# Optimization experiments

Hardware: AMD Instinct MI355X
Metric: run time of the kernel (lower is better)

Reference implementation:

```python
import jax, jax.numpy as jnp
import numpy as np

NUM_HEADS = 16

def setup_inputs() -> dict:
    key = jax.random.key(0)
    ks = jax.random.split(key, 5)
    b, c, w, h = 2, 1024, 48, 48
    sc = 0.02
    return {
        "x": jax.random.normal(ks[0], (b, c, w, h), jnp.float32),
        "Wqkv": jax.random.normal(ks[1], (3 * c, c), jnp.float32) * sc,
        "bqkv": jax.random.normal(ks[2], (3 * c,), jnp.float32) * sc,
        "Wo": jax.random.normal(ks[3], (c, c), jnp.float32) * sc,
        "bo": jax.random.normal(ks[4], (c,), jnp.float32) * sc,
    }

def reference(x, Wqkv, bqkv, Wo, bo):
    b, c, w, h = x.shape
    n = NUM_HEADS
    hd = c // n
    s = w * h
    # [b,c,w,h] -> tokens [b, s, c]
    xs = x.transpose(0, 2, 3, 1).reshape(b, s, c)
    qkv = xs @ Wqkv.T + bqkv                       # [b, s, 3c]
    # rearrange 'b s (three n hd) -> three b n s hd'
    qkv = qkv.reshape(b, s, 3, n, hd).transpose(2, 0, 3, 1, 4)
    q, k, v = qkv[0], qkv[1], qkv[2]               # [b, n, s, hd]
    score = jnp.einsum('bnqh,bnkh->bnqk', q, k) / jnp.sqrt(jnp.float32(hd))
    # module uses a soft causal mask: subtract 10000 above the diagonal
    mask = 10000.0 * jnp.triu(jnp.ones((s, s), dtype=score.dtype), k=1)
    attn = jax.nn.softmax(score - mask, axis=-1)   # [b, n, s, s]
    z = jnp.einsum('bnqk,bnkh->bqnh', attn, v).reshape(b, s, c)
    out = z @ Wo.T + bo                            # [b, s, c]
    return out.reshape(b, w, h, c).transpose(0, 3, 1, 2)
```

## Files before the change

### kernel.cpp

```cpp
#include <hip/hip_runtime.h>

typedef __bf16 bf16;
typedef __bf16 bf16x8 __attribute__((ext_vector_type(8)));
typedef float floatx4 __attribute__((ext_vector_type(4)));
typedef float floatx16 __attribute__((ext_vector_type(16)));

static constexpr int S = 2304;
static constexpr int C = 1024;
static constexpr int NHEAD = 16;
static constexpr int HDIM = 64;
static constexpr int BATCH = 2;
static constexpr float QSCALE = 0.18033688011112042f;
static constexpr int QACC0 = 512;
static constexpr int NACCQ = S - QACC0;
static constexpr int NPART = 3;

__global__ __launch_bounds__(256) void k_convert(const float* __restrict__ src,
                                                 bf16* __restrict__ dst, int n8) {
  int i = blockIdx.x * 256 + threadIdx.x;
  if (i >= n8) return;
  float4 a = *(const float4*)(src + (size_t)i * 8);
  float4 b = *(const float4*)(src + (size_t)i * 8 + 4);
  bf16x8 o;
  o[0] = (bf16)a.x; o[1] = (bf16)a.y; o[2] = (bf16)a.z; o[3] = (bf16)a.w;
  o[4] = (bf16)b.x; o[5] = (bf16)b.y; o[6] = (bf16)b.z; o[7] = (bf16)b.w;
  *(bf16x8*)(dst + (size_t)i * 8) = o;
}

__global__ __launch_bounds__(256) void k_transpose(const float* __restrict__ x,
                                                   bf16* __restrict__ xs) {
  __shared__ bf16 T[64 * 72];
  int c0 = blockIdx.x * 64, t0 = blockIdx.y * 64, b = blockIdx.z;
  int tid = threadIdx.x;
  const float* xb = x + (size_t)b * C * S;
#pragma unroll
  for (int it = 0; it < 4; ++it) {
    int idx = it * 256 + tid;
    int rc = idx >> 4, t4 = idx & 15;
    float4 v = *(const float4*)(xb + (size_t)(c0 + rc) * S + t0 + t4 * 4);
    T[(t4 * 4 + 0) * 72 + rc] = (bf16)v.x;
    T[(t4 * 4 + 1) * 72 + rc] = (bf16)v.y;
    T[(t4 * 4 + 2) * 72 + rc] = (bf16)v.z;
    T[(t4 * 4 + 3) * 72 + rc] = (bf16)v.w;
  }
  __syncthreads();
  bf16* xsb = xs + (size_t)b * S * C;
#pragma unroll
  for (int it = 0; it < 2; ++it) {
    int idx = it * 256 + tid;
    int rt = idx >> 3, c8 = idx & 7;
    bf16x8 v;
#pragma unroll
    for (int i = 0; i < 8; ++i) v[i] = T[rt * 72 + c8 * 8 + i];
    *(bf16x8*)(xsb + (size_t)(t0 + rt) * C + c0 + c8 * 8) = v;
  }
}

__device__ __forceinline__ void g2l16(const bf16* g, bf16* l) {
  __builtin_amdgcn_global_load_lds(
      (const __attribute__((address_space(1))) void*)g,
      (__attribute__((address_space(3))) void*)l, 16, 0, 0);
}

__device__ __forceinline__ unsigned cvtpk(float a, float b) {
  unsigned r;
  asm("v_cvt_pk_bf16_f32 %0, %1, %2" : "=v"(r) : "v"(a), "v"(b));
  return r;
}

__device__ __forceinline__ void pl32(unsigned& a, unsigned& b) {
  asm("v_permlane32_swap_b32 %0, %1" : "+v"(a), "+v"(b));
}

template <int EPI>
__global__ __launch_bounds__(256) void k_gemm_bt(const bf16* __restrict__ A,
                                                 const bf16* __restrict__ Bt,
                                                 const float* __restrict__ bias,
                                                 bf16* __restrict__ q,
                                                 bf16* __restrict__ k,
                                                 bf16* __restrict__ v,
                                                 float* __restrict__ outf) {
  constexpr int K = C;
  __shared__ bf16 As[128 * 64];
  __shared__ bf16 Bs[128 * 64];
  int tid = threadIdx.x;
  int w = tid >> 6, lane = tid & 63, ln = lane & 15, quad = lane >> 4;
  int m0 = blockIdx.y * 128, n0 = blockIdx.x * 128;
  int moff = (w >> 1) * 64, noff = (w & 1) * 64;
  floatx4 acc[4][4] = {};

  int sr[4], sc[4];
#pragma unroll
  for (int it = 0; it < 4; ++it) {
    int L = (it * 4 + w) * 64 + lane;
    sr[it] = L >> 3;
    sc[it] = (L & 7) ^ (sr[it] & 7);
  }

  for (int k0 = 0; k0 < K; k0 += 64) {
    __syncthreads();
#pragma unroll
    for (int it = 0; it < 4; ++it) {
      int cb = (it * 4 + w) * 64;
      g2l16(A + (size_t)(m0 + sr[it]) * K + k0 + sc[it] * 8, As + cb * 8);
      g2l16(Bt + (size_t)(n0 + sr[it]) * K + k0 + sc[it] * 8, Bs + cb * 8);
    }
    __syncthreads();
#pragma unroll
    for (int t = 0; t < 2; ++t) {
      bf16x8 af[4], bfr[4];
#pragma unroll
      for (int i = 0; i < 4; ++i) {
        int ra = moff + i * 16 + ln;
        af[i]  = *(const bf16x8*)(As + ra * 64 + (((t * 4 + quad) ^ (ra & 7))) * 8);
        int rb = noff + i * 16 + ln;
        bfr[i] = *(const bf16x8*)(Bs + rb * 64 + (((t * 4 + quad) ^ (rb & 7))) * 8);
      }
#pragma unroll
      for (int im = 0; im < 4; ++im)
#pragma unroll
        for (int in = 0; in < 4; ++in)
          acc[im][in] = __builtin_amdgcn_mfma_f32_16x16x32_bf16(
              af[im], bfr[in], acc[im][in], 0, 0, 0);
    }
  }

  int bidx = (m0 >= S) ? 1 : 0;
  if (EPI == 0) {
#pragma unroll
    for (int in = 0; in < 4; ++in) {
      int j = n0 + noff + in * 16 + ln;
      float bv = bias[j];
      int three = j >> 10;
      int head = (j >> 6) & 15;
      int hdi = j & 63;
#pragma unroll
      for (int im = 0; im < 4; ++im) {
        int mbase = m0 + moff + im * 16 + quad * 4;
        int tb = mbase - bidx * S;
        if (three == 2) {
          union { ushort4 u; bf16 h[4]; } P;
#pragma unroll
          for (int r = 0; r < 4; ++r) P.h[r] = (bf16)(acc[im][in][r] + bv);
          *(ushort4*)(v + ((size_t)(bidx * NHEAD + head) * HDIM + hdi) * S + tb) = P.u;
        } else if (three == 0) {
          bf16* dst = q + ((size_t)(bidx * NHEAD + head) * S + tb) * HDIM + hdi;
#pragma unroll
          for (int r = 0; r < 4; ++r)
            dst[(size_t)r * HDIM] = (bf16)((acc[im][in][r] + bv) * QSCALE);
        } else {
          bf16* dst = k + ((size_t)(bidx * NHEAD + head) * S + tb) * HDIM + hdi;
#pragma unroll
          for (int r = 0; r < 4; ++r) dst[(size_t)r * HDIM] = (bf16)(acc[im][in][r] + bv);
        }
      }
    }
  } else {
#pragma unroll
    for (int in = 0; in < 4; ++in) {
      int co = n0 + noff + in * 16 + ln;
      float bv = bias[co];
#pragma unroll
      for (int im = 0; im < 4; ++im) {
        int mbase = m0 + moff + im * 16 + quad * 4;
        int tb = mbase - bidx * S;
        float4 st;
        st.x = acc[im][in][0] + bv;
        st.y = acc[im][in][1] + bv;
        st.z = acc[im][in][2] + bv;
        st.w = acc[im][in][3] + bv;
        *(float4*)(outf + ((size_t)bidx * C + co) * S + tb) = st;
      }
    }
  }
}

__global__ __launch_bounds__(512) void k_attn_part(const bf16* __restrict__ Qg,
                                                   const bf16* __restrict__ Kg,
                                                   const bf16* __restrict__ Vtg,
                                                   bf16* __restrict__ z,
                                                   float* __restrict__ Oacc,
                                                   float* __restrict__ Lacc) {
  __shared__ bf16 Ks[3][64 * 64];
  __shared__ bf16 Vs[3][64 * 64];
  static const unsigned char QT[22] = {8,8,8,7,7,7,6,6,6,5,5,5,1,4,4,4,3,2,2,3,3,0};
  static const unsigned char LO[22] = {0,12,24,0,11,22,0,10,19,0,8,16,0,0,7,14,0,0,6,6,11,0};
  static const unsigned char HI[22] = {12,24,36,11,22,32,10,19,28,8,16,24,8,7,14,20,6,6,12,11,16,4};
  static const unsigned char PT[22] = {0,1,2,0,1,2,0,1,2,0,1,2,0,0,1,2,0,0,1,1,2,0};
  int i = blockIdx.x;
  int xcd = i & 7, j = i >> 3;
  int grp = j / 22, r = j % 22;
  int bh = xcd + 8 * grp;
  int qt = QT[r], lo = LO[r], hi = HI[r], part = PT[r];
  bool single = (qt <= 1);
  int b = bh >> 4, h = bh & 15;
  int tid = threadIdx.x;
  int w = tid >> 6, lane = tid & 63;
  int ql = lane & 31, hw = lane >> 5;
  int qw = qt * 256 + w * 32;
  int qg = qw + ql;
  int ktd = qw >> 6;

  const bf16* kb = Kg + (size_t)bh * S * HDIM;
  const bf16* vb = Vtg + (size_t)bh * HDIM * S;

  int s_row = tid >> 3;
  int s_c8 = (tid & 7) ^ (s_row & 7);
  size_t kOff = (size_t)s_row * HDIM + s_c8 * 8;
  size_t vOff = (size_t)s_row * S + s_c8 * 8;

  const bf16* qb = Qg + ((size_t)bh * S + qg) * HDIM + hw * 8;
  bf16x8 qf[4];
#pragma unroll
  for (int c = 0; c < 4; ++c) qf[c] = *(const bf16x8*)(qb + c * 16);

  float lsA = 0.f, lsB = 0.f;
  floatx16 o0 = {}, o1 = {};

  const bf16* kb0 = kb + (size_t)lo * 64 * HDIM;
  const bf16* vb0 = vb + (size_t)lo * 64;
  g2l16(kb0 + kOff, Ks[0] + tid * 8);
  g2l16(vb0 + vOff, Vs[0] + tid * 8);

  const bf16* kbn = kb0 + (size_t)64 * HDIM;
  const bf16* vbn = vb0 + 64;

  int qsw = ql & 7;
  int cur = 0;

#pragma unroll 1
  for (int kt = lo; kt < hi; ++kt) {
    int nxt = (cur == 2) ? 0 : cur + 1;
    if (kt + 1 < hi) {
      g2l16(kbn + kOff, Ks[nxt] + tid * 8);
      g2l16(vbn + vOff, Vs[nxt] + tid * 8);
      kbn += (size_t)64 * HDIM;
      vbn += 64;
      asm volatile("s_waitcnt vmcnt(2)" ::: "memory");
    } else {
      asm volatile("s_waitcnt vmcnt(0)" ::: "memory");
    }
    __builtin_amdgcn_s_barrier();

    const bf16* ksb = Ks[cur];
    const bf16* vsb = Vs[cur];
    cur = nxt;

    if (kt > ktd) continue;
    bool diag = (kt == ktd);

    floatx16 sa0 = {}, sa1 = {};
    __builtin_amdgcn_s_setprio(1);
#pragma unroll
    for (int c = 0; c < 4; ++c) {
      int c8 = ((2 * c + hw) ^ qsw) * 8;
      bf16x8 k0 = *(const bf16x8*)(ksb + ql * 64 + c8);
      bf16x8 k1 = *(const bf16x8*)(ksb + (32 + ql) * 64 + c8);
      sa0 = __builtin_amdgcn_mfma_f32_32x32x16_bf16(k0, qf[c], sa0, 0, 0, 0);
      sa1 = __builtin_amdgcn_mfma_f32_32x32x16_bf16(k1, qf[c], sa1, 0, 0, 0);
    }
    __builtin_amdgcn_s_setprio(0);

    unsigned pk0[8], pk1[8];
    if (!diag) {
#pragma unroll
      for (int t = 0; t < 8; ++t) {
        float a = exp2f(sa0[2 * t]), c2 = exp2f(sa0[2 * t + 1]);
        float d = exp2f(sa1[2 * t]), e = exp2f(sa1[2 * t + 1]);
        lsA += a + c2;
        lsB += d + e;
        pk0[t] = cvtpk(a, c2);
        pk1[t] = cvtpk(d, e);
      }
    } else {
      int qd = qg - kt * 64;
#pragma unroll
      for (int t = 0; t < 8; ++t) {
        int r0 = 2 * t, r1 = 2 * t + 1;
        int k0l = (r0 & 3) + 8 * (r0 >> 2) + 4 * hw;
        int k1l = (r1 & 3) + 8 * (r1 >> 2) + 4 * hw;
        float a = (k0l > qd) ? 0.f : exp2f(sa0[r0]);
        float c2 = (k1l > qd) ? 0.f : exp2f(sa0[r1]);
        float d = (32 + k0l > qd) ? 0.f : exp2f(sa1[r0]);
        float e = (32 + k1l > qd) ? 0.f : exp2f(sa1[r1]);
        lsA += a + c2;
        lsB += d + e;
        pk0[t] = cvtpk(a, c2);
        pk1[t] = cvtpk(d, e);
      }
    }

    __builtin_amdgcn_s_setprio(1);
#pragma unroll
    for (int ktc = 0; ktc < 4; ++ktc) {
      unsigned d0, d1, d2, d3;
      if (ktc == 0)      { d0 = pk0[0]; d1 = pk0[1]; d2 = pk0[2]; d3 = pk0[3]; }
      else if (ktc == 1) { d0 = pk0[4]; d1 = pk0[5]; d2 = pk0[6]; d3 = pk0[7]; }
      else if (ktc == 2) { d0 = pk1[0]; d1 = pk1[1]; d2 = pk1[2]; d3 = pk1[3]; }
      else               { d0 = pk1[4]; d1 = pk1[5]; d2 = pk1[6]; d3 = pk1[7]; }
      pl32(d0, d2);
      pl32(d1, d3);
      union { unsigned u[4]; bf16x8 v; } pf;
      pf.u[0] = d0; pf.u[1] = d1; pf.u[2] = d2; pf.u[3] = d3;
      int c8 = ((2 * ktc + hw) ^ qsw) * 8;
      bf16x8 v0 = *(const bf16x8*)(vsb + ql * 64 + c8);
      bf16x8 v1 = *(const bf16x8*)(vsb + (32 + ql) * 64 + c8);
      o0 = __builtin_amdgcn_mfma_f32_32x32x16_bf16(v0, pf.v, o0, 0, 0, 0);
      o1 = __builtin_amdgcn_mfma_f32_32x32x16_bf16(v1, pf.v, o1, 0, 0, 0);
    }
    __builtin_amdgcn_s_setprio(0);
  }

  float lsum = lsA + lsB;
  lsum += __shfl_xor(lsum, 32);

  if (single) {
    float inv = 1.f / lsum;
    bf16* dst = z + ((size_t)b * S + qg) * C + h * HDIM + 4 * hw;
#pragma unroll
    for (int hdblk = 0; hdblk < 2; ++hdblk) {
#pragma unroll
      for (int rg = 0; rg < 4; ++rg) {
        union { ushort4 u; bf16 hh[4]; } P;
#pragma unroll
        for (int jj = 0; jj < 4; ++jj) {
          float ov = hdblk ? o1[rg * 4 + jj] : o0[rg * 4 + jj];
          P.hh[jj] = (bf16)(ov * inv);
        }
        *(ushort4*)(dst + hdblk * 32 + rg * 8) = P.u;
      }
    }
  } else {
    int qa = qg - QACC0;
    float* ob = Oacc + (((size_t)part * 32 + bh) * NACCQ + qa) * 64;
    if (hw == 0) Lacc[((size_t)part * 32 + bh) * NACCQ + qa] = lsum;
#pragma unroll
    for (int g = 0; g < 4; ++g) {
      *(float4*)(ob + 4 * hw + 8 * g) =
          float4{o0[4 * g], o0[4 * g + 1], o0[4 * g + 2], o0[4 * g + 3]};
      *(float4*)(ob + 32 + 4 * hw + 8 * g) =
          float4{o1[4 * g], o1[4 * g + 1], o1[4 * g + 2], o1[4 * g + 3]};
    }
  }
}

__global__ __launch_bounds__(256) void k_norm(const float* __restrict__ Oacc,
                                              const float* __restrict__ Lacc,
                                              bf16* __restrict__ z) {
  int qt = blockIdx.x, bh = blockIdx.y;
  int b = bh >> 4, h = bh & 15;
  int tid = threadIdx.x;
  int q = tid >> 2;
  int seg = tid & 3;
  int qa = qt * 64 + q;
  bool np3 = (qa >= 256);
  float l = Lacc[(size_t)bh * NACCQ + qa] +
            Lacc[((size_t)32 + bh) * NACCQ + qa];
  if (np3) l += Lacc[((size_t)64 + bh) * NACCQ + qa];
  float inv = 1.f / l;
  const float* o0 = Oacc + ((size_t)bh * NACCQ + qa) * 64 + seg * 16;
  const float* o1 = Oacc + (((size_t)32 + bh) * NACCQ + qa) * 64 + seg * 16;
  const float* o2 = Oacc + (((size_t)64 + bh) * NACCQ + qa) * 64 + seg * 16;
  bf16* dst = z + ((size_t)b * S + QACC0 + qa) * C + h * HDIM + seg * 16;
#pragma unroll
  for (int half = 0; half < 2; ++half) {
    float4 a0 = *(const float4*)(o0 + half * 8);
    float4 a1 = *(const float4*)(o0 + half * 8 + 4);
    float4 b0 = *(const float4*)(o1 + half * 8);
    float4 b1 = *(const float4*)(o1 + half * 8 + 4);
    float s0 = a0.x + b0.x, s1 = a0.y + b0.y, s2 = a0.z + b0.z, s3 = a0.w + b0.w;
    float s4 = a1.x + b1.x, s5 = a1.y + b1.y, s6 = a1.z + b1.z, s7 = a1.w + b1.w;
    if (np3) {
      float4 c0 = *(const float4*)(o2 + half * 8);
      float4 c1 = *(const float4*)(o2 + half * 8 + 4);
      s0 += c0.x; s1 += c0.y; s2 += c0.z; s3 += c0.w;
      s4 += c1.x; s5 += c1.y; s6 += c1.z; s7 += c1.w;
    }
    bf16x8 o;
    o[0] = (bf16)(s0 * inv);
    o[1] = (bf16)(s1 * inv);
    o[2] = (bf16)(s2 * inv);
    o[3] = (bf16)(s3 * inv);
    o[4] = (bf16)(s4 * inv);
    o[5] = (bf16)(s5 * inv);
    o[6] = (bf16)(s6 * inv);
    o[7] = (bf16)(s7 * inv);
    *(bf16x8*)(dst + half * 8) = o;
  }
}

extern "C" void kernel_launch(void* const* d_in, const int* in_sizes, int n_in,
                              void* d_out, int out_size, void* d_ws, size_t ws_size,
                              hipStream_t stream) {
  const float* x    = (const float*)d_in[0];
  const float* Wqkv = (const float*)d_in[1];
  const float* bqkv = (const float*)d_in[2];
  const float* Wo   = (const float*)d_in[3];
  const float* bo   = (const float*)d_in[4];
  float* out = (float*)d_out;

  bf16* ws = (bf16*)d_ws;
  const size_t tok = (size_t)BATCH * S * C;
  bf16* xs   = ws;
  bf16* Qg   = ws + tok;
  bf16* Kg   = ws + 2 * tok;
  bf16* Vtg  = ws + 3 * tok;
  bf16* Wqb  = ws + 4 * tok;
  bf16* Wob  = Wqb + (size_t)3 * C * C;
  float* Oacc = (float*)(Wob + (size_t)C * C);
  float* Lacc = Oacc + (size_t)NPART * 32 * NACCQ * 64;
  bf16* z    = xs;

  k_convert<<<(3 * C * C / 8 + 255) / 256, 256, 0, stream>>>(Wqkv, Wqb, 3 * C * C / 8);
  k_convert<<<(C * C / 8 + 255) / 256, 256, 0, stream>>>(Wo, Wob, C * C / 8);
  k_transpose<<<dim3(C / 64, S / 64, BATCH), 256, 0, stream>>>(x, xs);
  k_gemm_bt<0><<<dim3(3 * C / 128, BATCH * S / 128), 256, 0, stream>>>(
      xs, Wqb, bqkv, Qg, Kg, Vtg, nullptr);
  k_attn_part<<<dim3(704), 512, 0, stream>>>(Qg, Kg, Vtg, z, Oacc, Lacc);
  k_norm<<<dim3(28, 32), 256, 0, stream>>>(Oacc, Lacc, z);
  k_gemm_bt<1><<<dim3(C / 128, BATCH * S / 128), 256, 0, stream>>>(
      z, Wob, bo, nullptr, nullptr, nullptr, out);
}
```

Measured before the change: 221.3 us.

## Double-buffer LDS tiles in projection GEMM with K-step of 32

Switches the QKV/output projection GEMM from a single 64-wide K tile with two barriers per step to double-buffered 32-wide K tiles. The next tile's global-to-LDS load is issued before the current tile's MFMAs, leaving one barrier per iteration. This aims to overlap memory latency with compute. In exchange the XOR swizzle is dropped, so LDS fragment reads with a 64-byte row stride may hit bank conflicts, and there are twice as many loop iterations.

Measured after the change: 232.6 us. 5.1% more time.

```diff
diff --git a/kernel.cpp b/kernel.cpp
--- a/kernel.cpp
+++ b/kernel.cpp
@@ -81,48 +81,53 @@
                                                  bf16* __restrict__ v,
                                                  float* __restrict__ outf) {
   constexpr int K = C;
-  __shared__ bf16 As[128 * 64];
-  __shared__ bf16 Bs[128 * 64];
+  constexpr int NT = K / 32;
+  __shared__ bf16 As[2][128 * 32];
+  __shared__ bf16 Bs[2][128 * 32];
   int tid = threadIdx.x;
   int w = tid >> 6, lane = tid & 63, ln = lane & 15, quad = lane >> 4;
   int m0 = blockIdx.y * 128, n0 = blockIdx.x * 128;
   int moff = (w >> 1) * 64, noff = (w & 1) * 64;
   floatx4 acc[4][4] = {};
 
-  int sr[4], sc[4];
-#pragma unroll
-  for (int it = 0; it < 4; ++it) {
-    int L = (it * 4 + w) * 64 + lane;
-    sr[it] = L >> 3;
-    sc[it] = (L & 7) ^ (sr[it] & 7);
-  }
-
-  for (int k0 = 0; k0 < K; k0 += 64) {
+  int s_row = tid >> 2, s_c = tid & 3;
+  const bf16* aSrc = A + (size_t)(m0 + s_row) * K + s_c * 8;
+  const bf16* bSrc = Bt + (size_t)(n0 + s_row) * K + s_c * 8;
+  const size_t rstep = (size_t)64 * K;
+
+  g2l16(aSrc, As[0] + tid * 8);
+  g2l16(aSrc + rstep, As[0] + (256 + tid) * 8);
+  g2l16(bSrc, Bs[0] + tid * 8);
+  g2l16(bSrc + rstep, Bs[0] + (256 + tid) * 8);
+  __syncthreads();
+
+  int cur = 0;
+#pragma unroll 2
+  for (int t = 0; t < NT; ++t) {
+    if (t + 1 < NT) {
+      const bf16* an = aSrc + (t + 1) * 32;
+      const bf16* bn = bSrc + (t + 1) * 32;
+      g2l16(an, As[cur ^ 1] + tid * 8);
+      g2l16(an + rstep, As[cur ^ 1] + (256 + tid) * 8);
+      g2l16(bn, Bs[cur ^ 1] + tid * 8);
+      g2l16(bn + rstep, Bs[cur ^ 1] + (256 + tid) * 8);
+    }
+    const bf16* as = As[cur];
+    const bf16* bs = Bs[cur];
+    bf16x8 af[4], bfr[4];
+#pragma unroll
+    for (int i = 0; i < 4; ++i) {
+      af[i]  = *(const bf16x8*)(as + (moff + i * 16 + ln) * 32 + quad * 8);
+      bfr[i] = *(const bf16x8*)(bs + (noff + i * 16 + ln) * 32 + quad * 8);
+    }
+#pragma unroll
+    for (int im = 0; im < 4; ++im)
+#pragma unroll
+      for (int in = 0; in < 4; ++in)
+        acc[im][in] = __builtin_amdgcn_mfma_f32_16x16x32_bf16(
+            af[im], bfr[in], acc[im][in], 0, 0, 0);
     __syncthreads();
-#pragma unroll
-    for (int it = 0; it < 4; ++it) {
-      int cb = (it * 4 + w) * 64;
-      g2l16(A + (size_t)(m0 + sr[it]) * K + k0 + sc[it] * 8, As + cb * 8);
-      g2l16(Bt + (size_t)(n0 + sr[it]) * K + k0 + sc[it] * 8, Bs + cb * 8);
-    }
-    __syncthreads();
-#pragma unroll
-    for (int t = 0; t < 2; ++t) {
-      bf16x8 af[4], bfr[4];
-#pragma unroll
-      for (int i = 0; i < 4; ++i) {
-        int ra = moff + i * 16 + ln;
-        af[i]  = *(const bf16x8*)(As + ra * 64 + (((t * 4 + quad) ^ (ra & 7))) * 8);
-        int rb = noff + i * 16 + ln;
-        bfr[i] = *(const bf16x8*)(Bs + rb * 64 + (((t * 4 + quad) ^ (rb & 7))) * 8);
-      }
-#pragma unroll
-      for (int im = 0; im < 4; ++im)
-#pragma unroll
-        for (int in = 0; in < 4; ++in)
-          acc[im][in] = __builtin_amdgcn_mfma_f32_16x16x32_bf16(
-              af[im], bfr[in], acc[im][in], 0, 0, 0);
-    }
+    cur ^= 1;
   }
 
   int bidx = (m0 >= S) ? 1 : 0;
```

## Load K/V fragments directly from global memory, drop shared-memory staging

Applied to the files above, without the earlier changes.

Removes the triple-buffered LDS staging of K and V tiles, along with the async global-to-LDS copies and per-tile barriers, in the attention partial kernel. Each wave now loads its K and V MFMA fragments straight from global memory into registers. It also stops the loop at the wave's own diagonal tile, so waves no longer run the barrier-only iterations past it. The 8 waves of a block no longer share one LDS copy, so global and L2 traffic goes up, loads are no longer prefetched ahead of compute, and register pressure rises.

After: 269.0 us. +21.6%, slower.

```diff
diff --git a/kernel.cpp b/kernel.cpp
--- a/kernel.cpp
+++ b/kernel.cpp
@@ -181,8 +181,6 @@
                                                    bf16* __restrict__ z,
                                                    float* __restrict__ Oacc,
                                                    float* __restrict__ Lacc) {
-  __shared__ bf16 Ks[3][64 * 64];
-  __shared__ bf16 Vs[3][64 * 64];
   static const unsigned char QT[22] = {8,8,8,7,7,7,6,6,6,5,5,5,1,4,4,4,3,2,2,3,3,0};
   static const unsigned char LO[22] = {0,12,24,0,11,22,0,10,19,0,8,16,0,0,7,14,0,0,6,6,11,0};
   static const unsigned char HI[22] = {12,24,36,11,22,32,10,19,28,8,16,24,8,7,14,20,6,6,12,11,16,4};
@@ -200,14 +198,13 @@
   int qw = qt * 256 + w * 32;
   int qg = qw + ql;
   int ktd = qw >> 6;
+  int myhi = (hi < ktd + 1) ? hi : ktd + 1;
 
   const bf16* kb = Kg + (size_t)bh * S * HDIM;
   const bf16* vb = Vtg + (size_t)bh * HDIM * S;
 
-  int s_row = tid >> 3;
-  int s_c8 = (tid & 7) ^ (s_row & 7);
-  size_t kOff = (size_t)s_row * HDIM + s_c8 * 8;
-  size_t vOff = (size_t)s_row * S + s_c8 * 8;
+  const bf16* kfb = kb + (size_t)ql * HDIM + hw * 8;
+  const bf16* vfb = vb + (size_t)ql * S + hw * 8;
 
   const bf16* qb = Qg + ((size_t)bh * S + qg) * HDIM + hw * 8;
   bf16x8 qf[4];
@@ -217,49 +214,33 @@
   float lsA = 0.f, lsB = 0.f;
   floatx16 o0 = {}, o1 = {};
 
-  const bf16* kb0 = kb + (size_t)lo * 64 * HDIM;
-  const bf16* vb0 = vb + (size_t)lo * 64;
-  g2l16(kb0 + kOff, Ks[0] + tid * 8);
-  g2l16(vb0 + vOff, Vs[0] + tid * 8);
-
-  const bf16* kbn = kb0 + (size_t)64 * HDIM;
-  const bf16* vbn = vb0 + 64;
-
-  int qsw = ql & 7;
-  int cur = 0;
-
 #pragma unroll 1
-  for (int kt = lo; kt < hi; ++kt) {
-    int nxt = (cur == 2) ? 0 : cur + 1;
-    if (kt + 1 < hi) {
-      g2l16(kbn + kOff, Ks[nxt] + tid * 8);
-      g2l16(vbn + vOff, Vs[nxt] + tid * 8);
-      kbn += (size_t)64 * HDIM;
-      vbn += 64;
-      asm volatile("s_waitcnt vmcnt(2)" ::: "memory");
-    } else {
-      asm volatile("s_waitcnt vmcnt(0)" ::: "memory");
-    }
-    __builtin_amdgcn_s_barrier();
-
-    const bf16* ksb = Ks[cur];
-    const bf16* vsb = Vs[cur];
-    cur = nxt;
-
-    if (kt > ktd) continue;
+  for (int kt = lo; kt < myhi; ++kt) {
     bool diag = (kt == ktd);
-
+    const bf16* kt0 = kfb + (size_t)kt * 64 * HDIM;
+    const bf16* vt0 = vfb + (size_t)kt * 64;
+
+    bf16x8 kf0[4], kf1[4];
+#pragma unroll
+    for (int c = 0; c < 4; ++c) {
+      kf0[c] = *(const bf16x8*)(kt0 + c * 16);
+      kf1[c] = *(const bf16x8*)(kt0 + (size_t)32 * HDIM + c * 16);
+    }
     floatx16 sa0 = {}, sa1 = {};
     __builtin_amdgcn_s_setprio(1);
 #pragma unroll
     for (int c = 0; c < 4; ++c) {
-      int c8 = ((2 * c + hw) ^ qsw) * 8;
-      bf16x8 k0 = *(const bf16x8*)(ksb + ql * 64 + c8);
-      bf16x8 k1 = *(const bf16x8*)(ksb + (32 + ql) * 64 + c8);
-      sa0 = __builtin_amdgcn_mfma_f32_32x32x16_bf16(k0, qf[c], sa0, 0, 0, 0);
-      sa1 = __builtin_amdgcn_mfma_f32_32x32x16_bf16(k1, qf[c], sa1, 0, 0, 0);
+      sa0 = __builtin_amdgcn_mfma_f32_32x32x16_bf16(kf0[c], qf[c], sa0, 0, 0, 0);
+      sa1 = __builtin_amdgcn_mfma_f32_32x32x16_bf16(kf1[c], qf[c], sa1, 0, 0, 0);
     }
     __builtin_amdgcn_s_setprio(0);
+
+    bf16x8 vf0[4], vf1[4];
+#pragma unroll
+    for (int ktc = 0; ktc < 4; ++ktc) {
+      vf0[ktc] = *(const bf16x8*)(vt0 + ktc * 16);
+      vf1[ktc] = *(const bf16x8*)(vt0 + (size_t)32 * S + ktc * 16);
+    }
 
     unsigned pk0[8], pk1[8];
     if (!diag) {
@@ -302,11 +283,8 @@
       pl32(d1, d3);
       union { unsigned u[4]; bf16x8 v; } pf;
       pf.u[0] = d0; pf.u[1] = d1; pf.u[2] = d2; pf.u[3] = d3;
-      int c8 = ((2 * ktc + hw) ^ qsw) * 8;
-      bf16x8 v0 = *(const bf16x8*)(vsb + ql * 64 + c8);
-      bf16x8 v1 = *(const bf16x8*)(vsb + (32 + ql) * 64 + c8);
-      o0 = __builtin_amdgcn_mfma_f32_32x32x16_bf16(v0, pf.v, o0, 0, 0, 0);
-      o1 = __builtin_amdgcn_mfma_f32_32x32x16_bf16(v1, pf.v, o1, 0, 0, 0);
+      o0 = __builtin_amdgcn_mfma_f32_32x32x16_bf16(vf0[ktc], pf.v, o0, 0, 0, 0);
+      o1 = __builtin_amdgcn_mfma_f32_32x32x16_bf16(vf1[ktc], pf.v, o1, 0, 0, 0);
     }
     __builtin_amdgcn_s_setprio(0);
   }
```

## Stage 128-key tiles with double buffering and rebalance attention split-K schedule

Applied to the files above, without the earlier changes.

The attention kernel now loads K/V in 128-key stages into two LDS buffers, where it previously used triple-buffered 64-key tiles. This halves the number of barriers and waitcnts per key. The work table is rebalanced to 18 entries per head group, so there are 576 blocks instead of 704, and query tiles up to 2 are now handled without splitting. QACC0 and the normalisation kernel's three-part threshold are adjusted to match. The cost is less prefetch depth, a waitcnt(0) at the end of each stage, and possibly worse load balance or occupancy from the larger LDS footprint.

Result: no change. 217.7 us (-1.6%).

```diff
diff --git a/kernel.cpp b/kernel.cpp
--- a/kernel.cpp
+++ b/kernel.cpp
@@ -11,7 +11,7 @@
 static constexpr int HDIM = 64;
 static constexpr int BATCH = 2;
 static constexpr float QSCALE = 0.18033688011112042f;
-static constexpr int QACC0 = 512;
+static constexpr int QACC0 = 768;
 static constexpr int NACCQ = S - QACC0;
 static constexpr int NPART = 3;
 
@@ -181,18 +181,18 @@
                                                    bf16* __restrict__ z,
                                                    float* __restrict__ Oacc,
                                                    float* __restrict__ Lacc) {
-  __shared__ bf16 Ks[3][64 * 64];
-  __shared__ bf16 Vs[3][64 * 64];
-  static const unsigned char QT[22] = {8,8,8,7,7,7,6,6,6,5,5,5,1,4,4,4,3,2,2,3,3,0};
-  static const unsigned char LO[22] = {0,12,24,0,11,22,0,10,19,0,8,16,0,0,7,14,0,0,6,6,11,0};
-  static const unsigned char HI[22] = {12,24,36,11,22,32,10,19,28,8,16,24,8,7,14,20,6,6,12,11,16,4};
-  static const unsigned char PT[22] = {0,1,2,0,1,2,0,1,2,0,1,2,0,0,1,2,0,0,1,1,2,0};
+  __shared__ bf16 Ks[2][128 * 64];
+  __shared__ bf16 Vs[2][64 * 128];
+  static const unsigned char QT[18] = {8,8,8,7,7,7,6,6,6,5,5,4,4,3,3,2,1,0};
+  static const unsigned char LO[18] = {0,12,24,0,12,22,0,10,20,0,12,0,10,0,8,0,0,0};
+  static const unsigned char HI[18] = {12,24,36,12,22,32,10,20,28,12,24,10,20,8,16,12,8,4};
+  static const unsigned char PT[18] = {0,1,2,0,1,2,0,1,2,0,1,0,1,0,1,0,0,0};
   int i = blockIdx.x;
   int xcd = i & 7, j = i >> 3;
-  int grp = j / 22, r = j % 22;
+  int r = j >> 2, grp = j & 3;
   int bh = xcd + 8 * grp;
   int qt = QT[r], lo = LO[r], hi = HI[r], part = PT[r];
-  bool single = (qt <= 1);
+  bool single = (qt <= 2);
   int b = bh >> 4, h = bh & 15;
   int tid = threadIdx.x;
   int w = tid >> 6, lane = tid & 63;
@@ -204,10 +204,14 @@
   const bf16* kb = Kg + (size_t)bh * S * HDIM;
   const bf16* vb = Vtg + (size_t)bh * HDIM * S;
 
-  int s_row = tid >> 3;
-  int s_c8 = (tid & 7) ^ (s_row & 7);
-  size_t kOff = (size_t)s_row * HDIM + s_c8 * 8;
-  size_t vOff = (size_t)s_row * S + s_c8 * 8;
+  int kr = tid >> 3;
+  int kc = (tid & 7) ^ (kr & 7);
+  size_t kOff1 = (size_t)kr * HDIM + kc * 8;
+  size_t kOff2 = kOff1 + (size_t)64 * HDIM;
+  int vr = tid >> 4;
+  int vc = (tid & 15) ^ (vr & 7);
+  size_t vOff1 = (size_t)vr * S + vc * 8;
+  size_t vOff2 = vOff1 + (size_t)32 * S;
 
   const bf16* qb = Qg + ((size_t)bh * S + qg) * HDIM + hw * 8;
   bf16x8 qf[4];
@@ -217,98 +221,110 @@
   float lsA = 0.f, lsB = 0.f;
   floatx16 o0 = {}, o1 = {};
 
+  int nst = (hi - lo) >> 1;
   const bf16* kb0 = kb + (size_t)lo * 64 * HDIM;
   const bf16* vb0 = vb + (size_t)lo * 64;
-  g2l16(kb0 + kOff, Ks[0] + tid * 8);
-  g2l16(vb0 + vOff, Vs[0] + tid * 8);
-
-  const bf16* kbn = kb0 + (size_t)64 * HDIM;
-  const bf16* vbn = vb0 + 64;
-
+  g2l16(kb0 + kOff1, Ks[0] + tid * 8);
+  g2l16(kb0 + kOff2, Ks[0] + (512 + tid) * 8);
+  g2l16(vb0 + vOff1, Vs[0] + tid * 8);
+  g2l16(vb0 + vOff2, Vs[0] + (512 + tid) * 8);
+  asm volatile("s_waitcnt vmcnt(0)" ::: "memory");
+  __builtin_amdgcn_s_barrier();
+
+  const bf16* kbn = kb0 + (size_t)128 * HDIM;
+  const bf16* vbn = vb0 + 128;
   int qsw = ql & 7;
   int cur = 0;
 
 #pragma unroll 1
-  for (int kt = lo; kt < hi; ++kt) {
-    int nxt = (cur == 2) ? 0 : cur + 1;
-    if (kt + 1 < hi) {
-      g2l16(kbn + kOff, Ks[nxt] + tid * 8);
-      g2l16(vbn + vOff, Vs[nxt] + tid * 8);
-      kbn += (size_t)64 * HDIM;
-      vbn += 64;
-      asm volatile("s_waitcnt vmcnt(2)" ::: "memory");
-    } else {
-      asm volatile("s_waitcnt vmcnt(0)" ::: "memory");
-    }
-    __builtin_amdgcn_s_barrier();
-
+  for (int st = 0; st < nst; ++st) {
+    if (st + 1 < nst) {
+      bf16* kd = Ks[cur ^ 1];
+      bf16* vd = Vs[cur ^ 1];
+      g2l16(kbn + kOff1, kd + tid * 8);
+      g2l16(kbn + kOff2, kd + (512 + tid) * 8);
+      g2l16(vbn + vOff1, vd + tid * 8);
+      g2l16(vbn + vOff2, vd + (512 + tid) * 8);
+      kbn += (size_t)128 * HDIM;
+      vbn += 128;
+    }
     const bf16* ksb = Ks[cur];
     const bf16* vsb = Vs[cur];
-    cur = nxt;
-
-    if (kt > ktd) continue;
-    bool diag = (kt == ktd);
-
-    floatx16 sa0 = {}, sa1 = {};
-    __builtin_amdgcn_s_setprio(1);
-#pragma unroll
-    for (int c = 0; c < 4; ++c) {
-      int c8 = ((2 * c + hw) ^ qsw) * 8;
-      bf16x8 k0 = *(const bf16x8*)(ksb + ql * 64 + c8);
-      bf16x8 k1 = *(const bf16x8*)(ksb + (32 + ql) * 64 + c8);
-      sa0 = __builtin_amdgcn_mfma_f32_32x32x16_bf16(k0, qf[c], sa0, 0, 0, 0);
-      sa1 = __builtin_amdgcn_mfma_f32_32x32x16_bf16(k1, qf[c], sa1, 0, 0, 0);
-    }
-    __builtin_amdgcn_s_setprio(0);
-
-    unsigned pk0[8], pk1[8];
-    if (!diag) {
-#pragma unroll
-      for (int t = 0; t < 8; ++t) {
-        float a = exp2f(sa0[2 * t]), c2 = exp2f(sa0[2 * t + 1]);
-        float d = exp2f(sa1[2 * t]), e = exp2f(sa1[2 * t + 1]);
-        lsA += a + c2;
-        lsB += d + e;
-        pk0[t] = cvtpk(a, c2);
-        pk1[t] = cvtpk(d, e);
-      }
-    } else {
-      int qd = qg - kt * 64;
-#pragma unroll
-      for (int t = 0; t < 8; ++t) {
-        int r0 = 2 * t, r1 = 2 * t + 1;
-        int k0l = (r0 & 3) + 8 * (r0 >> 2) + 4 * hw;
-        int k1l = (r1 & 3) + 8 * (r1 >> 2) + 4 * hw;
-        float a = (k0l > qd) ? 0.f : exp2f(sa0[r0]);
-        float c2 = (k1l > qd) ? 0.f : exp2f(sa0[r1]);
-        float d = (32 + k0l > qd) ? 0.f : exp2f(sa1[r0]);
-        float e = (32 + k1l > qd) ? 0.f : exp2f(sa1[r1]);
-        lsA += a + c2;
-        lsB += d + e;
-        pk0[t] = cvtpk(a, c2);
-        pk1[t] = cvtpk(d, e);
-      }
-    }
-
-    __builtin_amdgcn_s_setprio(1);
-#pragma unroll
-    for (int ktc = 0; ktc < 4; ++ktc) {
-      unsigned d0, d1, d2, d3;
-      if (ktc == 0)      { d0 = pk0[0]; d1 = pk0[1]; d2 = pk0[2]; d3 = pk0[3]; }
-      else if (ktc == 1) { d0 = pk0[4]; d1 = pk0[5]; d2 = pk0[6]; d3 = pk0[7]; }
-      else if (ktc == 2) { d0 = pk1[0]; d1 = pk1[1]; d2 = pk1[2]; d3 = pk1[3]; }
-      else               { d0 = pk1[4]; d1 = pk1[5]; d2 = pk1[6]; d3 = pk1[7]; }
-      pl32(d0, d2);
-      pl32(d1, d3);
-      union { unsigned u[4]; bf16x8 v; } pf;
-      pf.u[0] = d0; pf.u[1] = d1; pf.u[2] = d2; pf.u[3] = d3;
-      int c8 = ((2 * ktc + hw) ^ qsw) * 8;
-      bf16x8 v0 = *(const bf16x8*)(vsb + ql * 64 + c8);
-      bf16x8 v1 = *(const bf16x8*)(vsb + (32 + ql) * 64 + c8);
-      o0 = __builtin_amdgcn_mfma_f32_32x32x16_bf16(v0, pf.v, o0, 0, 0, 0);
-      o1 = __builtin_amdgcn_mfma_f32_32x32x16_bf16(v1, pf.v, o1, 0, 0, 0);
-    }
-    __builtin_amdgcn_s_setprio(0);
+    int ktbase = lo + 2 * st;
+
+#pragma unroll
+    for (int hh = 0; hh < 2; ++hh) {
+      int kt = ktbase + hh;
+      if (kt > ktd) continue;
+      bool diag = (kt == ktd);
+
+      floatx16 sa0 = {}, sa1 = {};
+      __builtin_amdgcn_s_setprio(1);
+#pragma unroll
+      for (int c = 0; c < 4; ++c) {
+        int c8 = ((2 * c + hw) ^ qsw) * 8;
+        bf16x8 k0 = *(const bf16x8*)(ksb + (hh * 64 + ql) * 64 + c8);
+        bf16x8 k1 = *(const bf16x8*)(ksb + (hh * 64 + 32 + ql) * 64 + c8);
+        sa0 = __builtin_amdgcn_mfma_f32_32x32x16_bf16(k0, qf[c], sa0, 0, 0, 0);
+        sa1 = __builtin_amdgcn_mfma_f32_32x32x16_bf16(k1, qf[c], sa1, 0, 0, 0);
+      }
+      __builtin_amdgcn_s_setprio(0);
+
+      unsigned pk0[8], pk1[8];
+      if (!diag) {
+#pragma unroll
+        for (int t = 0; t < 8; ++t) {
+          float a = exp2f(sa0[2 * t]), c2 = exp2f(sa0[2 * t + 1]);
+          float d = exp2f(sa1[2 * t]), e = exp2f(sa1[2 * t + 1]);
+          lsA += a + c2;
+          lsB += d + e;
+          pk0[t] = cvtpk(a, c2);
+          pk1[t] = cvtpk(d, e);
+        }
+      } else {
+        int qd = qg - kt * 64;
+#pragma unroll
+        for (int t = 0; t < 8; ++t) {
+          int r0 = 2 * t, r1 = 2 * t + 1;
+          int k0l = (r0 & 3) + 8 * (r0 >> 2) + 4 * hw;
+          int k1l = (r1 & 3) + 8 * (r1 >> 2) + 4 * hw;
+          float a = (k0l > qd) ? 0.f : exp2f(sa0[r0]);
+          float c2 = (k1l > qd) ? 0.f : exp2f(sa0[r1]);
+          float d = (32 + k0l > qd) ? 0.f : exp2f(sa1[r0]);
+          float e = (32 + k1l > qd) ? 0.f : exp2f(sa1[r1]);
+          lsA += a + c2;
+          lsB += d + e;
+          pk0[t] = cvtpk(a, c2);
+          pk1[t] = cvtpk(d, e);
+        }
+      }
+
+      __builtin_amdgcn_s_setprio(1);
+#pragma unroll
+      for (int ktc = 0; ktc < 4; ++ktc) {
+        unsigned d0, d1, d2, d3;
+        if (ktc == 0)      { d0 = pk0[0]; d1 = pk0[1]; d2 = pk0[2]; d3 = pk0[3]; }
+        else if (ktc == 1) { d0 = pk0[4]; d1 = pk0[5]; d2 = pk0[6]; d3 = pk0[7]; }
+        else if (ktc == 2) { d0 = pk1[0]; d1 = pk1[1]; d2 = pk1[2]; d3 = pk1[3]; }
+        else               { d0 = pk1[4]; d1 = pk1[5]; d2 = pk1[6]; d3 = pk1[7]; }
+        pl32(d0, d2);
+        pl32(d1, d3);
+        union { unsigned u[4]; bf16x8 v; } pf;
+        pf.u[0] = d0; pf.u[1] = d1; pf.u[2] = d2; pf.u[3] = d3;
+        int c16 = hh * 8 + ((2 * ktc + hw) ^ qsw);
+        bf16x8 v0 = *(const bf16x8*)(vsb + ql * 128 + c16 * 8);
+        bf16x8 v1 = *(const bf16x8*)(vsb + (32 + ql) * 128 + c16 * 8);
+        o0 = __builtin_amdgcn_mfma_f32_32x32x16_bf16(v0, pf.v, o0, 0, 0, 0);
+        o1 = __builtin_amdgcn_mfma_f32_32x32x16_bf16(v1, pf.v, o1, 0, 0, 0);
+      }
+      __builtin_amdgcn_s_setprio(0);
+    }
+
+    if (st + 1 < nst) {
+      asm volatile("s_waitcnt vmcnt(0)" ::: "memory");
+      __builtin_amdgcn_s_barrier();
+      cur ^= 1;
+    }
   }
 
   float lsum = lsA + lsB;
@@ -353,7 +369,7 @@
   int q = tid >> 2;
   int seg = tid & 3;
   int qa = qt * 64 + q;
-  bool np3 = (qa >= 256);
+  bool np3 = (qa >= 768);
   float l = Lacc[(size_t)bh * NACCQ + qa] +
             Lacc[((size_t)32 + bh) * NACCQ + qa];
   if (np3) l += Lacc[((size_t)64 + bh) * NACCQ + qa];
@@ -416,8 +432,8 @@
   k_transpose<<<dim3(C / 64, S / 64, BATCH), 256, 0, stream>>>(x, xs);
   k_gemm_bt<0><<<dim3(3 * C / 128, BATCH * S / 128), 256, 0, stream>>>(
       xs, Wqb, bqkv, Qg, Kg, Vtg, nullptr);
-  k_attn_part<<<dim3(704), 512, 0, stream>>>(Qg, Kg, Vtg, z, Oacc, Lacc);
-  k_norm<<<dim3(28, 32), 256, 0, stream>>>(Oacc, Lacc, z);
+  k_attn_part<<<dim3(576), 512, 0, stream>>>(Qg, Kg, Vtg, z, Oacc, Lacc);
+  k_norm<<<dim3(24, 32), 256, 0, stream>>>(Oacc, Lacc, z);
   k_gemm_bt<1><<<dim3(C / 128, BATCH * S / 128), 256, 0, stream>>>(
       z, Wob, bo, nullptr, nullptr, nullptr, out);
 }
```
